# Kernel optimization log

Hardware: AMD Instinct MI355X
Metric: run time of the kernel (lower is better)

Reference implementation:

```python
import jax, jax.numpy as jnp
import numpy as np

N, E, B = 150000, 600000, 1024
F_IN, F_HID = 78, 312          # 78 * 2**output_dim_power_0(=2)
OUT_DIM = 128
L, VOCAB, EMB = 1000, 26, 128  # num_features_xt+1 = 26 embedding rows
NF, KS = 8, 8                  # 2**n_filters_power, 2**kernel_size_power
CONV_FLAT = NF * (EMB - KS + 1)  # 8*121 = 968
K_HOPS = 2
SLOPE = 0.01                   # torch leaky_relu default

def _lin(k, i, o):
    s = 1.0 / np.sqrt(i)
    kw, kb = jax.random.split(k)
    return (jax.random.uniform(kw, (i, o), jnp.float32, -s, s),
            jax.random.uniform(kb, (o,), jnp.float32, -s, s))

def setup_inputs() -> dict:
    key = jax.random.key(0)
    ks = jax.random.split(key, 12)
    x = jax.random.normal(ks[0], (N, F_IN), jnp.float32)
    edge_index = jax.random.randint(ks[1], (2, E), 0, N)
    batch = (jnp.arange(N) * B) // N            # sorted graph ids, all B graphs nonempty
    target = jax.random.randint(ks[2], (B, L), 0, VOCAB)
    sgc_w, sgc_b = _lin(ks[3], F_IN, F_HID)
    fcg1_w, fcg1_b = _lin(ks[4], F_HID, OUT_DIM)
    emb_table = jax.random.normal(ks[5], (VOCAB, EMB), jnp.float32)
    sc = 1.0 / np.sqrt(L * KS)
    conv_w = jax.random.uniform(ks[6], (NF, L, KS), jnp.float32, -sc, sc)  # OIW
    conv_b = jax.random.uniform(ks[7], (NF,), jnp.float32, -sc, sc)
    fcxt_w, fcxt_b = _lin(ks[8], CONV_FLAT, OUT_DIM)
    fc1_w, fc1_b = _lin(ks[9], 2 * OUT_DIM, 1024)
    fc2_w, fc2_b = _lin(ks[10], 1024, 512)
    out_w, out_b = _lin(ks[11], 512, 1)
    return dict(x=x, sgc_w=sgc_w, sgc_b=sgc_b, fcg1_w=fcg1_w, fcg1_b=fcg1_b,
                emb_table=emb_table, conv_w=conv_w, conv_b=conv_b,
                fcxt_w=fcxt_w, fcxt_b=fcxt_b, fc1_w=fc1_w, fc1_b=fc1_b,
                fc2_w=fc2_w, fc2_b=fc2_b, out_w=out_w, out_b=out_b,
                edge_index=edge_index, batch=batch, target=target)

def reference(x, sgc_w, sgc_b, fcg1_w, fcg1_b, emb_table, conv_w, conv_b,
              fcxt_w, fcxt_b, fc1_w, fc1_b, fc2_w, fc2_b, out_w, out_b,
              edge_index, batch, target):
    # --- SGConv: K-hop symmetric-normalized propagation with self-loops, then linear ---
    loop = jnp.arange(N)
    src = jnp.concatenate([edge_index[0], loop])
    dst = jnp.concatenate([edge_index[1], loop])
    deg = jax.ops.segment_sum(jnp.ones_like(src, jnp.float32), dst, num_segments=N)
    dinv = jnp.where(deg > 0, jax.lax.rsqrt(deg), 0.0)
    norm = (dinv[src] * dinv[dst])[:, None]
    h = x
    for _ in range(K_HOPS):
        h = jax.ops.segment_sum(h[src] * norm, dst, num_segments=N)  # [N, F]
    h = jax.nn.leaky_relu(h @ sgc_w + sgc_b, SLOPE)                  # [N, 312]
    # --- global max pool per graph + fc_g1 ---
    g = jax.ops.segment_max(h, batch, num_segments=B)                # [B, 312]
    g = jax.nn.leaky_relu(g @ fcg1_w + fcg1_b, SLOPE)                # [B, 128]
    # --- protein branch: embed -> Conv1d(in=1000) over embed axis -> flatten -> fc ---
    emb = emb_table[target]                                          # [B, 1000, 128]
    conv = jax.lax.conv_general_dilated(emb, conv_w, (1,), 'VALID',
                                        dimension_numbers=('NCW', 'OIW', 'NCW'))
    conv = conv + conv_b[None, :, None]                              # [B, 8, 121]
    xt = conv.reshape(B, CONV_FLAT) @ fcxt_w + fcxt_b                # [B, 128]
    # --- head ---
    xc = jnp.concatenate([g, xt], axis=1)                            # [B, 256]
    xc = jax.nn.relu(xc @ fc1_w + fc1_b)
    xc = jax.nn.relu(xc @ fc2_w + fc2_b)
    return xc @ out_w + out_b                                        # [B, 1]
```

## Files before the change

### kernel.cpp

```cpp
#include <hip/hip_runtime.h>

#define N_NODES 150000
#define N_EDGES 600000
#define BATCH   1024
#define F_IN    78
#define F_HID   312
#define OUT_DIMW 128
#define SEQ_L   1000
#define VOCAB   26
#define EMB     128
#define NF      8
#define KS      8
#define CONV_WO 121
#define CONV_FLAT 968
#define SK      208
#define SLOPE   0.01f
#define KEY_NEGMAX ((int)0x80800000)
#define SCAN_NBLK ((N_NODES + 255) / 256)

#define NT   20
#define BSW_HALF (3 * NT * 64 * 8)
#define M_PAD 150016
#define GM_BLKS (M_PAD / 128 * 2)
#define GM_CHUNK (GM_BLKS / 8)

#define WSW_HALF 65536

typedef __attribute__((ext_vector_type(8))) short bf8;
typedef __attribute__((ext_vector_type(4))) float f4;

__device__ __forceinline__ short f2bf(float f) {
  unsigned u = __float_as_uint(f);
  return (short)((u + 0x7fffu + ((u >> 16) & 1u)) >> 16);
}
__device__ __forceinline__ float bf2f(short h) {
  return __uint_as_float(((unsigned)(unsigned short)h) << 16);
}

__device__ __forceinline__ int fkey(float v) {
  int i = __float_as_int(v);
  return i >= 0 ? i : (i ^ 0x7fffffff);
}
__device__ __forceinline__ float fdec(int k) {
  return __int_as_float(k >= 0 ? k : (k ^ 0x7fffffff));
}

__global__ void k_zero_i(int* __restrict__ p, int n) {
  int i = blockIdx.x * blockDim.x + threadIdx.x;
  if (i < n) p[i] = 0;
}

__global__ void k_deg(const int* __restrict__ dst, int* __restrict__ deg) {
  int e = blockIdx.x * blockDim.x + threadIdx.x;
  if (e < N_EDGES) atomicAdd(&deg[dst[e]], 1);
}

__global__ void k_dinv(const int* __restrict__ deg, float* __restrict__ dinv) {
  int i = blockIdx.x * blockDim.x + threadIdx.x;
  if (i < N_NODES) dinv[i] = rsqrtf((float)(deg[i] + 1));
}

__global__ __launch_bounds__(256) void k_scan1(const int* __restrict__ deg, int* __restrict__ rowptr,
                                               int* __restrict__ bsum) {
  __shared__ int s[256];
  int tid = threadIdx.x;
  int i = blockIdx.x * 256 + tid;
  int v = (i < N_NODES) ? deg[i] : 0;
  s[tid] = v;
  __syncthreads();
  int x = v;
  for (int o = 1; o < 256; o <<= 1) {
    int t = (tid >= o) ? s[tid - o] : 0;
    __syncthreads();
    x += t; s[tid] = x;
    __syncthreads();
  }
  if (i < N_NODES) rowptr[i] = x - v;
  if (tid == 255) bsum[blockIdx.x] = x;
}

__global__ __launch_bounds__(1024) void k_scan2(int* __restrict__ bsum) {
  __shared__ int s[1024];
  int tid = threadIdx.x;
  int v = (tid < SCAN_NBLK) ? bsum[tid] : 0;
  s[tid] = v;
  __syncthreads();
  int x = v;
  for (int o = 1; o < 1024; o <<= 1) {
    int t = (tid >= o) ? s[tid - o] : 0;
    __syncthreads();
    x += t; s[tid] = x;
    __syncthreads();
  }
  if (tid < SCAN_NBLK) bsum[tid] = x - v;
}

__global__ __launch_bounds__(256) void k_scan3(int* __restrict__ rowptr, const int* __restrict__ bsum,
                                               int* __restrict__ cnt) {
  int i = blockIdx.x * 256 + threadIdx.x;
  if (i < N_NODES) { rowptr[i] += bsum[blockIdx.x]; cnt[i] = 0; }
  if (i == 0) rowptr[N_NODES] = N_EDGES;
}

__global__ void k_fillcsr(const int* __restrict__ src, const int* __restrict__ dst,
                          const int* __restrict__ rowptr, int* __restrict__ cnt,
                          int* __restrict__ csr) {
  int e = blockIdx.x * blockDim.x + threadIdx.x;
  if (e < N_EDGES) {
    int d = dst[e];
    int pos = rowptr[d] + atomicAdd(&cnt[d], 1);
    csr[pos] = src[e];
  }
}

template<int HOP1>
__global__ __launch_bounds__(256) void k_pull(const int* __restrict__ rowptr,
                        const int* __restrict__ csr, const float* __restrict__ dinv,
                        const float* __restrict__ p, void* __restrict__ outv) {
  int dv = (int)((blockIdx.x * 256 + threadIdx.x) >> 6);
  if (dv >= N_NODES) return;
  int d = __builtin_amdgcn_readfirstlane(dv);
  int lane = threadIdx.x & 63;
  int j0 = rowptr[d], j1 = rowptr[d + 1];
  bool act = lane < 39;
  float dd = dinv[d];
  float2 aA = make_float2(0.f, 0.f), aB = aA, aC = aA, aD = aA;
  if (act) {
    float2 v = ((const float2*)(p + (size_t)d * F_IN))[lane];
    float c0 = HOP1 ? dd : 1.f;
    aA.x = c0 * v.x; aA.y = c0 * v.y;
  }
  int j = j0;
  for (; j + 3 < j1; j += 4) {
    int s0 = csr[j], s1 = csr[j + 1], s2 = csr[j + 2], s3 = csr[j + 3];
    float c0 = HOP1 ? dinv[s0] : 1.f, c1 = HOP1 ? dinv[s1] : 1.f;
    float c2 = HOP1 ? dinv[s2] : 1.f, c3 = HOP1 ? dinv[s3] : 1.f;
    if (act) {
      float2 u0 = ((const float2*)(p + (size_t)s0 * F_IN))[lane];
      float2 u1 = ((const float2*)(p + (size_t)s1 * F_IN))[lane];
      float2 u2 = ((const float2*)(p + (size_t)s2 * F_IN))[lane];
      float2 u3 = ((const float2*)(p + (size_t)s3 * F_IN))[lane];
      aA.x += c0 * u0.x; aA.y += c0 * u0.y;
      aB.x += c1 * u1.x; aB.y += c1 * u1.y;
      aC.x += c2 * u2.x; aC.y += c2 * u2.y;
      aD.x += c3 * u3.x; aD.y += c3 * u3.y;
    }
  }
  if (j + 1 < j1) {
    int s0 = csr[j], s1 = csr[j + 1];
    float c0 = HOP1 ? dinv[s0] : 1.f, c1 = HOP1 ? dinv[s1] : 1.f;
    if (act) {
      float2 u0 = ((const float2*)(p + (size_t)s0 * F_IN))[lane];
      float2 u1 = ((const float2*)(p + (size_t)s1 * F_IN))[lane];
      aA.x += c0 * u0.x; aA.y += c0 * u0.y;
      aB.x += c1 * u1.x; aB.y += c1 * u1.y;
    }
    j += 2;
  }
  if (j < j1) {
    int s0 = csr[j];
    float c0 = HOP1 ? dinv[s0] : 1.f;
    if (act) {
      float2 u0 = ((const float2*)(p + (size_t)s0 * F_IN))[lane];
      aC.x += c0 * u0.x; aC.y += c0 * u0.y;
    }
  }
  if (HOP1) {
    if (act) {
      float cs = dd * dd;
      ((float2*)((float*)outv + (size_t)d * F_IN))[lane] =
          make_float2(cs * (aA.x + aB.x + aC.x + aD.x), cs * (aA.y + aB.y + aC.y + aD.y));
    }
  } else {
    if (lane < 48) {
      float vx = dd * (aA.x + aB.x + aC.x + aD.x);
      float vy = dd * (aA.y + aB.y + aC.y + aD.y);
      short hx = f2bf(vx); short lx = f2bf(vx - bf2f(hx));
      short hy = f2bf(vy); short ly = f2bf(vy - bf2f(hy));
      int t = d >> 4, mrow = d & 15;
      int ksi = lane >> 4;
      int quad = (lane & 15) >> 2;
      int jj = (2 * lane) & 7;
      size_t base = (((size_t)(t * 3 + ksi) * 2) * 64 + quad * 16 + mrow) * 8 + jj;
      short* o = (short*)outv;
      *(unsigned*)(o + base) =
          (unsigned)(unsigned short)hx | ((unsigned)(unsigned short)hy << 16);
      *(unsigned*)(o + base + 512) =
          (unsigned)(unsigned short)lx | ((unsigned)(unsigned short)ly << 16);
    }
  }
}

__global__ __launch_bounds__(256) void k_gemm_sk(const float* __restrict__ A, const float* __restrict__ B,
                        float* __restrict__ Cp, int M, int N, int K, int kc) {
  __shared__ float As[16][33];
  __shared__ float Bs[16][68];
  int bm = blockIdx.x * 32, bn = blockIdx.y * 64;
  int k0s = blockIdx.z * kc;
  int k1s = min(K, k0s + kc);
  int tid = threadIdx.x;
  int tx = tid & 15, ty = tid >> 4;
  float acc[2][4] = {};
  for (int k0 = k0s; k0 < k1s; k0 += 16) {
    {
      int i2 = tid * 2;
      int m = i2 >> 4, k = i2 & 15;
      float2 av = make_float2(0.f, 0.f);
      const float* Ap = A + (size_t)(bm + m) * K + k0 + k;
      if (k0 + k + 1 < k1s)      av = *(const float2*)Ap;
      else if (k0 + k < k1s)     av.x = Ap[0];
      As[k][m] = av.x; As[k + 1][m] = av.y;
    }
    {
      int i4 = tid * 4;
      int kr = i4 >> 6, n = i4 & 63;
      float4 bv = make_float4(0.f, 0.f, 0.f, 0.f);
      if (k0 + kr < k1s) bv = *(const float4*)(B + (size_t)(k0 + kr) * N + bn + n);
      *(float4*)&Bs[kr][n] = bv;
    }
    __syncthreads();
#pragma unroll
    for (int kk = 0; kk < 16; kk++) {
      float a0 = As[kk][ty * 2], a1 = As[kk][ty * 2 + 1];
      float4 b = *(const float4*)&Bs[kk][tx * 4];
      acc[0][0] += a0 * b.x; acc[0][1] += a0 * b.y; acc[0][2] += a0 * b.z; acc[0][3] += a0 * b.w;
      acc[1][0] += a1 * b.x; acc[1][1] += a1 * b.y; acc[1][2] += a1 * b.z; acc[1][3] += a1 * b.w;
    }
    __syncthreads();
  }
#pragma unroll
  for (int im = 0; im < 2; im++) {
    int m = bm + ty * 2 + im;
    float4 v = make_float4(acc[im][0], acc[im][1], acc[im][2], acc[im][3]);
    *(float4*)(Cp + ((size_t)blockIdx.z * M + m) * N + bn + tx * 4) = v;
  }
}

template<int ACT>
__global__ void k_sumact(const float* __restrict__ Cp, int S, const float* __restrict__ bias,
                         float* __restrict__ C, int nshift, int ldc, int coff) {
  int i = blockIdx.x * 256 + threadIdx.x;
  int MN = gridDim.x * 256;
  int m = i >> nshift, n = i & ((1 << nshift) - 1);
  float s = 0.f;
  for (int t = 0; t < S; t++) s += Cp[(size_t)t * MN + i];
  s += bias[n];
  if (ACT == 1) s = fmaxf(s, 0.f);
  if (ACT == 2) s = s > 0.f ? s : SLOPE * s;
  C[(size_t)m * ldc + coff + n] = s;
}

__global__ void k_bprep(const float* __restrict__ B, short* __restrict__ Bsw,
                        int* __restrict__ gkeys) {
  int i = blockIdx.x * 256 + threadIdx.x;
  if (i < BATCH * F_HID) gkeys[i] = KEY_NEGMAX;
  if (i >= BSW_HALF) return;
  int j = i & 7;
  int lane = (i >> 3) & 63;
  int rest = i >> 9;
  int nt = rest % NT, ksi = rest / NT;
  int n = nt * 16 + (lane & 15);
  int k = ksi * 32 + (lane >> 4) * 8 + j;
  float v = (k < F_IN && n < F_HID) ? B[k * F_HID + n] : 0.f;
  short h = f2bf(v);
  Bsw[i] = h;
  Bsw[BSW_HALF + i] = f2bf(v - bf2f(h));
}

__global__ void k_wprep(const float* __restrict__ conv_w, short* __restrict__ Wsw) {
  int i = blockIdx.x * 256 + threadIdx.x;
  if (i >= WSW_HALF) return;
  int j = i & 7;
  int lane = (i >> 3) & 63;
  int rest = i >> 9;
  int nt = rest & 3, ks = rest >> 2;
  int fk = nt * 16 + (lane & 15);
  int l = ks * 32 + (lane >> 4) * 8 + j;
  float v = (l < SEQ_L) ? conv_w[(fk >> 3) * (SEQ_L * KS) + l * KS + (fk & 7)] : 0.f;
  short h = f2bf(v);
  Wsw[i] = h;
  Wsw[WSW_HALF + i] = f2bf(v - bf2f(h));
}

__global__ __launch_bounds__(512) void k_gemm_max(const short* __restrict__ hA,
                           const short* __restrict__ Bsw,
                           const float* __restrict__ bias, int* __restrict__ gkeys) {
  __shared__ int red[2 * F_HID];
  int tid = threadIdx.x;

  int bid = blockIdx.x;
  int swz = (bid & 7) * GM_CHUNK + (bid >> 3);
  int mIdx = swz >> 1, nh2 = swz & 1;
  int m0 = mIdx * 128;

  int w = tid >> 6, lane = tid & 63;
  int mq = w & 3, nh = w >> 2;
  int ntb = (nh2 * 2 + nh) * 5;
  int mrow = lane & 15, quad = lane >> 4;

  int t0 = (m0 + mq * 32) >> 4;
  const short* apb = hA + (size_t)t0 * 3072 + (size_t)lane * 8;
  bf8 ah[2][3], al[2][3];
#pragma unroll
  for (int mi = 0; mi < 2; mi++)
#pragma unroll
    for (int ksi = 0; ksi < 3; ksi++) {
      const short* ap = apb + (size_t)(mi * 3 + ksi) * 1024;
      ah[mi][ksi] = *(const bf8*)ap;
      al[mi][ksi] = *(const bf8*)(ap + 512);
    }

  for (int i = tid; i < 2 * F_HID; i += 512) red[i] = KEY_NEGMAX;
  __syncthreads();

  f4 acc[2][5];
#pragma unroll
  for (int mi = 0; mi < 2; mi++)
#pragma unroll
    for (int j = 0; j < 5; j++) acc[mi][j] = (f4)0.f;

  const short* bbase = Bsw + ((size_t)ntb * 64 + lane) * 8;

#pragma unroll
  for (int ksi = 0; ksi < 3; ksi++) {
    const short* bh = bbase + (size_t)ksi * (NT * 512);
    const short* bl = bh + BSW_HALF;
#pragma unroll
    for (int j = 0; j < 5; j++) {
      bf8 bhv = *(const bf8*)(bh + j * 512);
      bf8 blv = *(const bf8*)(bl + j * 512);
#pragma unroll
      for (int mi = 0; mi < 2; mi++) {
        acc[mi][j] = __builtin_amdgcn_mfma_f32_16x16x32_bf16(ah[mi][ksi], bhv, acc[mi][j], 0, 0, 0);
        acc[mi][j] = __builtin_amdgcn_mfma_f32_16x16x32_bf16(al[mi][ksi], bhv, acc[mi][j], 0, 0, 0);
        acc[mi][j] = __builtin_amdgcn_mfma_f32_16x16x32_bf16(ah[mi][ksi], blv, acc[mi][j], 0, 0, 0);
      }
    }
  }

  int g0 = (int)(((long long)m0 * BATCH) / N_NODES);
#pragma unroll
  for (int mi = 0; mi < 2; mi++) {
    int mgrp = m0 + mq * 32 + mi * 16;
    int gg  = (int)(((long long)mgrp * BATCH) / N_NODES);
    int bndg = (int)((((long long)(gg + 1)) * N_NODES + BATCH - 1) / BATCH);
    int s = gg - g0;
    int mb = mgrp + quad * 4;
    if (bndg >= mgrp + 16 && mgrp + 16 <= N_NODES) {
#pragma unroll
      for (int j = 0; j < 5; j++) {
        int n = (ntb + j) * 16 + mrow;
        bool nok = n < F_HID;
        float bn = nok ? bias[n] : 0.f;
        float v0 = acc[mi][j][0] + bn; v0 = v0 > 0.f ? v0 : SLOPE * v0;
        float v1 = acc[mi][j][1] + bn; v1 = v1 > 0.f ? v1 : SLOPE * v1;
        float v2 = acc[mi][j][2] + bn; v2 = v2 > 0.f ? v2 : SLOPE * v2;
        float v3 = acc[mi][j][3] + bn; v3 = v3 > 0.f ? v3 : SLOPE * v3;
        float mx = fmaxf(fmaxf(v0, v1), fmaxf(v2, v3));
        mx = fmaxf(mx, __shfl_xor(mx, 16, 64));
        mx = fmaxf(mx, __shfl_xor(mx, 32, 64));
        if (quad == 0 && nok) atomicMax(&red[s * F_HID + n], fkey(mx));
      }
    } else {
#pragma unroll
      for (int j = 0; j < 5; j++) {
        int n = (ntb + j) * 16 + mrow;
        bool nok = n < F_HID;
        float bn = nok ? bias[n] : 0.f;
        float mx0 = -3.4e38f, mx1 = -3.4e38f;
#pragma unroll
        for (int r = 0; r < 4; r++) {
          int m = mb + r;
          if (m >= N_NODES) continue;
          float v = acc[mi][j][r] + bn;
          v = v > 0.f ? v : SLOPE * v;
          if (m >= bndg) mx1 = fmaxf(mx1, v); else mx0 = fmaxf(mx0, v);
        }
        mx0 = fmaxf(mx0, __shfl_xor(mx0, 16, 64));
        mx0 = fmaxf(mx0, __shfl_xor(mx0, 32, 64));
        mx1 = fmaxf(mx1, __shfl_xor(mx1, 16, 64));
        mx1 = fmaxf(mx1, __shfl_xor(mx1, 32, 64));
        if (quad == 0 && nok) {
          if (mx0 > -3.3e38f) atomicMax(&red[s * F_HID + n], fkey(mx0));
          if (mx1 > -3.3e38f && s == 0) atomicMax(&red[F_HID + n], fkey(mx1));
        }
      }
    }
  }
  __syncthreads();
  for (int i = tid; i < 2 * F_HID; i += 512) {
    int flag = i / F_HID, n = i - flag * F_HID;
    int g = g0 + flag;
    int key = red[i];
    if (g < BATCH && key != KEY_NEGMAX)
      atomicMax(&gkeys[g * F_HID + n], key);
  }
}

__global__ void k_decode(const int* __restrict__ gkeys, float* __restrict__ g, int n) {
  int i = blockIdx.x * blockDim.x + threadIdx.x;
  if (i < n) g[i] = fdec(gkeys[i]);
}

__global__ __launch_bounds__(256) void k_sbuild(const int* __restrict__ target,
                        const short* __restrict__ Wsw, float* __restrict__ Sg) {
  __shared__ int tl[4][1024];
  int tid = threadIdx.x;
  int w = tid >> 6, lane = tid & 63;
  int b = blockIdx.x * 4 + w;

  const int4* tg4 = (const int4*)(target + (size_t)b * SEQ_L);
  int4* tl4 = (int4*)&tl[w][0];
  for (int i = lane; i < 250; i += 64) tl4[i] = tg4[i];
  if (lane < 24) tl[w][1000 + lane] = -1;
  __syncthreads();

  int mrow = lane & 15, quad = lane >> 4;
  f4 acc[2][4];
#pragma unroll
  for (int mt = 0; mt < 2; mt++)
#pragma unroll
    for (int nt = 0; nt < 4; nt++) acc[mt][nt] = (f4)0.f;

  const short one = (short)0x3F80;
#pragma unroll 4
  for (int ks = 0; ks < 32; ks++) {
    int l0 = ks * 32 + quad * 8;
    int4 t0 = *(const int4*)&tl[w][l0];
    int4 t1 = *(const int4*)&tl[w][l0 + 4];
    int tv[8] = {t0.x, t0.y, t0.z, t0.w, t1.x, t1.y, t1.z, t1.w};
    bf8 a0, a1;
#pragma unroll
    for (int j = 0; j < 8; j++) {
      a0[j] = (tv[j] == mrow) ? one : (short)0;
      a1[j] = (tv[j] == mrow + 16) ? one : (short)0;
    }
    const short* bp = Wsw + ((size_t)(ks * 4) * 64 + lane) * 8;
    bf8 bh[4], bl[4];
#pragma unroll
    for (int nt = 0; nt < 4; nt++) {
      bh[nt] = *(const bf8*)(bp + nt * 512);
      bl[nt] = *(const bf8*)(bp + nt * 512 + WSW_HALF);
    }
#pragma unroll
    for (int nt = 0; nt < 4; nt++) {
      acc[0][nt] = __builtin_amdgcn_mfma_f32_16x16x32_bf16(a0, bh[nt], acc[0][nt], 0, 0, 0);
      acc[1][nt] = __builtin_amdgcn_mfma_f32_16x16x32_bf16(a1, bh[nt], acc[1][nt], 0, 0, 0);
    }
#pragma unroll
    for (int nt = 0; nt < 4; nt++) {
      acc[0][nt] = __builtin_amdgcn_mfma_f32_16x16x32_bf16(a0, bl[nt], acc[0][nt], 0, 0, 0);
      acc[1][nt] = __builtin_amdgcn_mfma_f32_16x16x32_bf16(a1, bl[nt], acc[1][nt], 0, 0, 0);
    }
  }

#pragma unroll
  for (int mt = 0; mt < 2; mt++)
#pragma unroll
    for (int nt = 0; nt < 4; nt++) {
      int fk = nt * 16 + mrow;
      float* sp = Sg + ((size_t)b * NF + (fk >> 3)) * SK + (fk & 7);
#pragma unroll
      for (int r = 0; r < 4; r++) {
        int v = mt * 16 + quad * 4 + r;
        if (v < VOCAB) sp[v * KS] = acc[mt][nt][r];
      }
    }
}

__global__ __launch_bounds__(256) void k_conv(const float* __restrict__ Sg, const float* __restrict__ emb,
                       const float* __restrict__ conv_b, float* __restrict__ convo) {
  __shared__ float Asub[32][SK];
  __shared__ float Etab[VOCAB * EMB];
  int r0 = blockIdx.x * 32;
  int tid = threadIdx.x;
  float* Af = &Asub[0][0];
  for (int i = tid; i < VOCAB * EMB; i += 256) Etab[i] = emb[i];
  for (int i = tid; i < 32 * SK; i += 256) Af[i] = Sg[(size_t)r0 * SK + i];
  __syncthreads();
  int w = tid & 127;
  int rg = tid >> 7;
  if (w < CONV_WO) {
    float acc[16] = {};
    for (int vk4 = 0; vk4 < SK; vk4 += 4) {
      int v0 = vk4 >> 3, k0 = vk4 & 7;
      float e0 = Etab[v0 * EMB + w + k0];
      float e1 = Etab[v0 * EMB + w + k0 + 1];
      float e2 = Etab[v0 * EMB + w + k0 + 2];
      float e3 = Etab[v0 * EMB + w + k0 + 3];
#pragma unroll
      for (int r = 0; r < 16; r++) {
        float4 a4 = *(const float4*)&Asub[rg * 16 + r][vk4];
        acc[r] += a4.x * e0 + a4.y * e1 + a4.z * e2 + a4.w * e3;
      }
    }
#pragma unroll
    for (int r = 0; r < 16; r++) {
      int row = r0 + rg * 16 + r;
      convo[(size_t)row * CONV_WO + w] = acc[r] + conv_b[row & 7];
    }
  }
}

__global__ void k_out(const float* __restrict__ a2, const float* __restrict__ w,
                      const float* __restrict__ b, float* __restrict__ out) {
  int row = (blockIdx.x * blockDim.x + threadIdx.x) >> 6;
  int lane = threadIdx.x & 63;
  if (row >= BATCH) return;
  const float* ar = a2 + (size_t)row * 512;
  float s = 0.f;
  for (int j = lane; j < 512; j += 64) s += ar[j] * w[j];
  for (int o = 32; o > 0; o >>= 1) s += __shfl_down(s, o, 64);
  if (lane == 0) out[row] = s + b[0];
}

extern "C" void kernel_launch(void* const* d_in, const int* in_sizes, int n_in,
                              void* d_out, int out_size, void* d_ws, size_t ws_size,
                              hipStream_t stream) {
  const float* x      = (const float*)d_in[0];
  const float* sgc_w  = (const float*)d_in[1];
  const float* sgc_b  = (const float*)d_in[2];
  const float* fcg1_w = (const float*)d_in[3];
  const float* fcg1_b = (const float*)d_in[4];
  const float* emb    = (const float*)d_in[5];
  const float* conv_w = (const float*)d_in[6];
  const float* conv_b = (const float*)d_in[7];
  const float* fcxt_w = (const float*)d_in[8];
  const float* fcxt_b = (const float*)d_in[9];
  const float* fc1_w  = (const float*)d_in[10];
  const float* fc1_b  = (const float*)d_in[11];
  const float* fc2_w  = (const float*)d_in[12];
  const float* fc2_b  = (const float*)d_in[13];
  const float* out_w  = (const float*)d_in[14];
  const float* out_b  = (const float*)d_in[15];
  const int* edge     = (const int*)d_in[16];
  const int* target   = (const int*)d_in[18];
  float* out = (float*)d_out;

  char* ws = (char*)d_ws;
  size_t off = 0;
  auto take = [&](size_t bytes) {
    void* p = ws + off;
    off += (bytes + 255) & ~(size_t)255;
    return p;
  };
  int*      deg    = (int*)     take((size_t)N_NODES * 4);
  float*    dinv   = (float*)   take((size_t)N_NODES * 4);
  int*      rowptr = (int*)     take((size_t)(N_NODES + 1) * 4);
  int*      bsum   = (int*)     take((size_t)SCAN_NBLK * 4);
  int*      cnt    = (int*)     take((size_t)N_NODES * 4);
  int*      csr    = (int*)     take((size_t)N_EDGES * 4);
  short*    hA     = (short*)   take((size_t)M_PAD * 192 * 2);
  float*    hB     = (float*)   take((size_t)N_NODES * F_IN * 4);
  short*    Bsw    = (short*)   take((size_t)2 * BSW_HALF * 2);
  short*    Wsw    = (short*)   take((size_t)2 * WSW_HALF * 2);
  int*      gkeys  = (int*)     take((size_t)BATCH * F_HID * 4);
  float*    gbuf   = (float*)   take((size_t)BATCH * F_HID * 4);
  float*    Sg     = (float*)   take((size_t)BATCH * NF * SK * 4);
  float*    convo  = (float*)   take((size_t)BATCH * NF * CONV_WO * 4);
  float*    xc     = (float*)   take((size_t)BATCH * 256 * 4);
  float*    a1     = (float*)   take((size_t)BATCH * 1024 * 4);
  float*    a2     = (float*)   take((size_t)BATCH * 512 * 4);
  float*    psum   = hB;

  const int* esrc = edge;
  const int* edst = edge + N_EDGES;

  k_zero_i<<<(N_NODES + 255) / 256, 256, 0, stream>>>(deg, N_NODES);
  k_deg<<<(N_EDGES + 255) / 256, 256, 0, stream>>>(edst, deg);
  k_dinv<<<(N_NODES + 255) / 256, 256, 0, stream>>>(deg, dinv);
  k_scan1<<<SCAN_NBLK, 256, 0, stream>>>(deg, rowptr, bsum);
  k_scan2<<<1, 1024, 0, stream>>>(bsum);
  k_scan3<<<SCAN_NBLK, 256, 0, stream>>>(rowptr, bsum, cnt);
  k_fillcsr<<<(N_EDGES + 255) / 256, 256, 0, stream>>>(esrc, edst, rowptr, cnt, csr);

  k_pull<1><<<(N_NODES * 64 + 255) / 256, 256, 0, stream>>>(rowptr, csr, dinv, x, hB);
  k_pull<0><<<(N_NODES * 64 + 255) / 256, 256, 0, stream>>>(rowptr, csr, dinv, hB, hA);

  k_bprep<<<(BATCH * F_HID + 255) / 256, 256, 0, stream>>>(sgc_w, Bsw, gkeys);
  k_gemm_max<<<GM_BLKS, 512, 0, stream>>>(hA, Bsw, sgc_b, gkeys);
  k_decode<<<(BATCH * F_HID + 255) / 256, 256, 0, stream>>>(gkeys, gbuf, BATCH * F_HID);

  {
    dim3 g(BATCH / 32, OUT_DIMW / 64, 4);
    k_gemm_sk<<<g, 256, 0, stream>>>(gbuf, fcg1_w, psum, BATCH, OUT_DIMW, F_HID, 80);
    k_sumact<2><<<(BATCH * OUT_DIMW) / 256, 256, 0, stream>>>(psum, 4, fcg1_b, xc, 7, 256, 0);
  }

  k_wprep<<<WSW_HALF / 256, 256, 0, stream>>>(conv_w, Wsw);
  k_sbuild<<<BATCH / 4, 256, 0, stream>>>(target, Wsw, Sg);
  k_conv<<<(BATCH * NF) / 32, 256, 0, stream>>>(Sg, emb, conv_b, convo);
  {
    dim3 g(BATCH / 32, OUT_DIMW / 64, 8);
    k_gemm_sk<<<g, 256, 0, stream>>>(convo, fcxt_w, psum, BATCH, OUT_DIMW, CONV_FLAT, 128);
    k_sumact<0><<<(BATCH * OUT_DIMW) / 256, 256, 0, stream>>>(psum, 8, fcxt_b, xc, 7, 256, OUT_DIMW);
  }

  {
    dim3 g(BATCH / 32, 1024 / 64, 2);
    k_gemm_sk<<<g, 256, 0, stream>>>(xc, fc1_w, psum, BATCH, 1024, 256, 128);
    k_sumact<1><<<(BATCH * 1024) / 256, 256, 0, stream>>>(psum, 2, fc1_b, a1, 10, 1024, 0);
  }
  {
    dim3 g(BATCH / 32, 512 / 64, 4);
    k_gemm_sk<<<g, 256, 0, stream>>>(a1, fc2_w, psum, BATCH, 512, 1024, 256);
    k_sumact<1><<<(BATCH * 512) / 256, 256, 0, stream>>>(psum, 4, fc2_b, a2, 9, 512, 0);
  }
  k_out<<<(BATCH * 64) / 256, 256, 0, stream>>>(a2, out_w, out_b, out);
}
```

Before: 494.7 us.

## Fuse small prep kernels, pad hop-1 rows, fold decode and fc1 bias/relu

```diff
diff --git a/kernel.cpp b/kernel.cpp
--- a/kernel.cpp
+++ b/kernel.cpp
@@ -4,6 +4,7 @@
 #define N_EDGES 600000
 #define BATCH   1024
 #define F_IN    78
+#define HB_S    80
 #define F_HID   312
 #define OUT_DIMW 128
 #define SEQ_L   1000
@@ -55,13 +56,8 @@
   if (e < N_EDGES) atomicAdd(&deg[dst[e]], 1);
 }
 
-__global__ void k_dinv(const int* __restrict__ deg, float* __restrict__ dinv) {
-  int i = blockIdx.x * blockDim.x + threadIdx.x;
-  if (i < N_NODES) dinv[i] = rsqrtf((float)(deg[i] + 1));
-}
-
 __global__ __launch_bounds__(256) void k_scan1(const int* __restrict__ deg, int* __restrict__ rowptr,
-                                               int* __restrict__ bsum) {
+                                               int* __restrict__ bsum, float* __restrict__ dinv) {
   __shared__ int s[256];
   int tid = threadIdx.x;
   int i = blockIdx.x * 256 + tid;
@@ -75,7 +71,10 @@
     x += t; s[tid] = x;
     __syncthreads();
   }
-  if (i < N_NODES) rowptr[i] = x - v;
+  if (i < N_NODES) {
+    rowptr[i] = x - v;
+    dinv[i] = rsqrtf((float)(v + 1));
+  }
   if (tid == 255) bsum[blockIdx.x] = x;
 }
 
@@ -117,6 +116,7 @@
 __global__ __launch_bounds__(256) void k_pull(const int* __restrict__ rowptr,
                         const int* __restrict__ csr, const float* __restrict__ dinv,
                         const float* __restrict__ p, void* __restrict__ outv) {
+  const int RS = HOP1 ? F_IN : HB_S;
   int dv = (int)((blockIdx.x * 256 + threadIdx.x) >> 6);
   if (dv >= N_NODES) return;
   int d = __builtin_amdgcn_readfirstlane(dv);
@@ -126,7 +126,7 @@
   float dd = dinv[d];
   float2 aA = make_float2(0.f, 0.f), aB = aA, aC = aA, aD = aA;
   if (act) {
-    float2 v = ((const float2*)(p + (size_t)d * F_IN))[lane];
+    float2 v = ((const float2*)(p + (size_t)d * RS))[lane];
     float c0 = HOP1 ? dd : 1.f;
     aA.x = c0 * v.x; aA.y = c0 * v.y;
   }
@@ -136,10 +136,10 @@
     float c0 = HOP1 ? dinv[s0] : 1.f, c1 = HOP1 ? dinv[s1] : 1.f;
     float c2 = HOP1 ? dinv[s2] : 1.f, c3 = HOP1 ? dinv[s3] : 1.f;
     if (act) {
-      float2 u0 = ((const float2*)(p + (size_t)s0 * F_IN))[lane];
-      float2 u1 = ((const float2*)(p + (size_t)s1 * F_IN))[lane];
-      float2 u2 = ((const float2*)(p + (size_t)s2 * F_IN))[lane];
-      float2 u3 = ((const float2*)(p + (size_t)s3 * F_IN))[lane];
+      float2 u0 = ((const float2*)(p + (size_t)s0 * RS))[lane];
+      float2 u1 = ((const float2*)(p + (size_t)s1 * RS))[lane];
+      float2 u2 = ((const float2*)(p + (size_t)s2 * RS))[lane];
+      float2 u3 = ((const float2*)(p + (size_t)s3 * RS))[lane];
       aA.x += c0 * u0.x; aA.y += c0 * u0.y;
       aB.x += c1 * u1.x; aB.y += c1 * u1.y;
       aC.x += c2 * u2.x; aC.y += c2 * u2.y;
@@ -150,8 +150,8 @@
     int s0 = csr[j], s1 = csr[j + 1];
     float c0 = HOP1 ? dinv[s0] : 1.f, c1 = HOP1 ? dinv[s1] : 1.f;
     if (act) {
-      float2 u0 = ((const float2*)(p + (size_t)s0 * F_IN))[lane];
-      float2 u1 = ((const float2*)(p + (size_t)s1 * F_IN))[lane];
+      float2 u0 = ((const float2*)(p + (size_t)s0 * RS))[lane];
+      float2 u1 = ((const float2*)(p + (size_t)s1 * RS))[lane];
       aA.x += c0 * u0.x; aA.y += c0 * u0.y;
       aB.x += c1 * u1.x; aB.y += c1 * u1.y;
     }
@@ -161,14 +161,14 @@
     int s0 = csr[j];
     float c0 = HOP1 ? dinv[s0] : 1.f;
     if (act) {
-      float2 u0 = ((const float2*)(p + (size_t)s0 * F_IN))[lane];
+      float2 u0 = ((const float2*)(p + (size_t)s0 * RS))[lane];
       aC.x += c0 * u0.x; aC.y += c0 * u0.y;
     }
   }
   if (HOP1) {
     if (act) {
       float cs = dd * dd;
-      ((float2*)((float*)outv + (size_t)d * F_IN))[lane] =
+      ((float2*)((float*)outv + (size_t)d * HB_S))[lane] =
           make_float2(cs * (aA.x + aB.x + aC.x + aD.x), cs * (aA.y + aB.y + aC.y + aD.y));
     }
   } else {
@@ -191,6 +191,7 @@
   }
 }
 
+template<int DEC>
 __global__ __launch_bounds__(256) void k_gemm_sk(const float* __restrict__ A, const float* __restrict__ B,
                         float* __restrict__ Cp, int M, int N, int K, int kc) {
   __shared__ float As[16][33];
@@ -209,6 +210,7 @@
       const float* Ap = A + (size_t)(bm + m) * K + k0 + k;
       if (k0 + k + 1 < k1s)      av = *(const float2*)Ap;
       else if (k0 + k < k1s)     av.x = Ap[0];
+      if (DEC) { av.x = fdec(__float_as_int(av.x)); av.y = fdec(__float_as_int(av.y)); }
       As[k][m] = av.x; As[k + 1][m] = av.y;
     }
     {
@@ -233,6 +235,54 @@
     int m = bm + ty * 2 + im;
     float4 v = make_float4(acc[im][0], acc[im][1], acc[im][2], acc[im][3]);
     *(float4*)(Cp + ((size_t)blockIdx.z * M + m) * N + bn + tx * 4) = v;
+  }
+}
+
+template<int ACT>
+__global__ __launch_bounds__(256) void k_gemm_dw(const float* __restrict__ A, const float* __restrict__ B,
+                        const float* __restrict__ bias, float* __restrict__ C, int M, int N, int K) {
+  __shared__ float As[16][33];
+  __shared__ float Bs[16][68];
+  int bm = blockIdx.x * 32, bn = blockIdx.y * 64;
+  int tid = threadIdx.x;
+  int tx = tid & 15, ty = tid >> 4;
+  float acc[2][4] = {};
+  for (int k0 = 0; k0 < K; k0 += 16) {
+    {
+      int i2 = tid * 2;
+      int m = i2 >> 4, k = i2 & 15;
+      float2 av = make_float2(0.f, 0.f);
+      const float* Ap = A + (size_t)(bm + m) * K + k0 + k;
+      if (k0 + k + 1 < K)      av = *(const float2*)Ap;
+      else if (k0 + k < K)     av.x = Ap[0];
+      As[k][m] = av.x; As[k + 1][m] = av.y;
+    }
+    {
+      int i4 = tid * 4;
+      int kr = i4 >> 6, n = i4 & 63;
+      float4 bv = make_float4(0.f, 0.f, 0.f, 0.f);
+      if (k0 + kr < K) bv = *(const float4*)(B + (size_t)(k0 + kr) * N + bn + n);
+      *(float4*)&Bs[kr][n] = bv;
+    }
+    __syncthreads();
+#pragma unroll
+    for (int kk = 0; kk < 16; kk++) {
+      float a0 = As[kk][ty * 2], a1 = As[kk][ty * 2 + 1];
+      float4 b = *(const float4*)&Bs[kk][tx * 4];
+      acc[0][0] += a0 * b.x; acc[0][1] += a0 * b.y; acc[0][2] += a0 * b.z; acc[0][3] += a0 * b.w;
+      acc[1][0] += a1 * b.x; acc[1][1] += a1 * b.y; acc[1][2] += a1 * b.z; acc[1][3] += a1 * b.w;
+    }
+    __syncthreads();
+  }
+  float4 bv = *(const float4*)&bias[bn + tx * 4];
+#pragma unroll
+  for (int im = 0; im < 2; im++) {
+    int m = bm + ty * 2 + im;
+    float4 v = make_float4(acc[im][0] + bv.x, acc[im][1] + bv.y, acc[im][2] + bv.z, acc[im][3] + bv.w);
+    if (ACT == 1) { v.x = fmaxf(v.x, 0.f); v.y = fmaxf(v.y, 0.f); v.z = fmaxf(v.z, 0.f); v.w = fmaxf(v.w, 0.f); }
+    if (ACT == 2) { v.x = v.x > 0.f ? v.x : SLOPE * v.x; v.y = v.y > 0.f ? v.y : SLOPE * v.y;
+                    v.z = v.z > 0.f ? v.z : SLOPE * v.z; v.w = v.w > 0.f ? v.w : SLOPE * v.w; }
+    *(float4*)(C + (size_t)m * N + bn + tx * 4) = v;
   }
 }
 
@@ -250,36 +300,35 @@
   C[(size_t)m * ldc + coff + n] = s;
 }
 
-__global__ void k_bprep(const float* __restrict__ B, short* __restrict__ Bsw,
-                        int* __restrict__ gkeys) {
+__global__ void k_prep(const float* __restrict__ B, short* __restrict__ Bsw,
+                       const float* __restrict__ conv_w, short* __restrict__ Wsw,
+                       int* __restrict__ gkeys) {
   int i = blockIdx.x * 256 + threadIdx.x;
   if (i < BATCH * F_HID) gkeys[i] = KEY_NEGMAX;
-  if (i >= BSW_HALF) return;
-  int j = i & 7;
-  int lane = (i >> 3) & 63;
-  int rest = i >> 9;
-  int nt = rest % NT, ksi = rest / NT;
-  int n = nt * 16 + (lane & 15);
-  int k = ksi * 32 + (lane >> 4) * 8 + j;
-  float v = (k < F_IN && n < F_HID) ? B[k * F_HID + n] : 0.f;
-  short h = f2bf(v);
-  Bsw[i] = h;
-  Bsw[BSW_HALF + i] = f2bf(v - bf2f(h));
-}
-
-__global__ void k_wprep(const float* __restrict__ conv_w, short* __restrict__ Wsw) {
-  int i = blockIdx.x * 256 + threadIdx.x;
-  if (i >= WSW_HALF) return;
-  int j = i & 7;
-  int lane = (i >> 3) & 63;
-  int rest = i >> 9;
-  int nt = rest & 3, ks = rest >> 2;
-  int fk = nt * 16 + (lane & 15);
-  int l = ks * 32 + (lane >> 4) * 8 + j;
-  float v = (l < SEQ_L) ? conv_w[(fk >> 3) * (SEQ_L * KS) + l * KS + (fk & 7)] : 0.f;
-  short h = f2bf(v);
-  Wsw[i] = h;
-  Wsw[WSW_HALF + i] = f2bf(v - bf2f(h));
+  if (i < BSW_HALF) {
+    int j = i & 7;
+    int lane = (i >> 3) & 63;
+    int rest = i >> 9;
+    int nt = rest % NT, ksi = rest / NT;
+    int n = nt * 16 + (lane & 15);
+    int k = ksi * 32 + (lane >> 4) * 8 + j;
+    float v = (k < F_IN && n < F_HID) ? B[k * F_HID + n] : 0.f;
+    short h = f2bf(v);
+    Bsw[i] = h;
+    Bsw[BSW_HALF + i] = f2bf(v - bf2f(h));
+  }
+  if (i < WSW_HALF) {
+    int j = i & 7;
+    int lane = (i >> 3) & 63;
+    int rest = i >> 9;
+    int nt = rest & 3, ks = rest >> 2;
+    int fk = nt * 16 + (lane & 15);
+    int l = ks * 32 + (lane >> 4) * 8 + j;
+    float v = (l < SEQ_L) ? conv_w[(fk >> 3) * (SEQ_L * KS) + l * KS + (fk & 7)] : 0.f;
+    short h = f2bf(v);
+    Wsw[i] = h;
+    Wsw[WSW_HALF + i] = f2bf(v - bf2f(h));
+  }
 }
 
 __global__ __launch_bounds__(512) void k_gemm_max(const short* __restrict__ hA,
@@ -395,11 +444,6 @@
     if (g < BATCH && key != KEY_NEGMAX)
       atomicMax(&gkeys[g * F_HID + n], key);
   }
-}
-
-__global__ void k_decode(const int* __restrict__ gkeys, float* __restrict__ g, int n) {
-  int i = blockIdx.x * blockDim.x + threadIdx.x;
-  if (i < n) g[i] = fdec(gkeys[i]);
 }
 
 __global__ __launch_bounds__(256) void k_sbuild(const int* __restrict__ target,
@@ -551,11 +595,10 @@
   int*      cnt    = (int*)     take((size_t)N_NODES * 4);
   int*      csr    = (int*)     take((size_t)N_EDGES * 4);
   short*    hA     = (short*)   take((size_t)M_PAD * 192 * 2);
-  float*    hB     = (float*)   take((size_t)N_NODES * F_IN * 4);
+  float*    hB     = (float*)   take((size_t)N_NODES * HB_S * 4);
   short*    Bsw    = (short*)   take((size_t)2 * BSW_HALF * 2);
   short*    Wsw    = (short*)   take((size_t)2 * WSW_HALF * 2);
   int*      gkeys  = (int*)     take((size_t)BATCH * F_HID * 4);
-  float*    gbuf   = (float*)   take((size_t)BATCH * F_HID * 4);
   float*    Sg     = (float*)   take((size_t)BATCH * NF * SK * 4);
   float*    convo  = (float*)   take((size_t)BATCH * NF * CONV_WO * 4);
   float*    xc     = (float*)   take((size_t)BATCH * 256 * 4);
@@ -568,42 +611,39 @@
 
   k_zero_i<<<(N_NODES + 255) / 256, 256, 0, stream>>>(deg, N_NODES);
   k_deg<<<(N_EDGES + 255) / 256, 256, 0, stream>>>(edst, deg);
-  k_dinv<<<(N_NODES + 255) / 256, 256, 0, stream>>>(deg, dinv);
-  k_scan1<<<SCAN_NBLK, 256, 0, stream>>>(deg, rowptr, bsum);
+  k_scan1<<<SCAN_NBLK, 256, 0, stream>>>(deg, rowptr, bsum, dinv);
   k_scan2<<<1, 1024, 0, stream>>>(bsum);
   k_scan3<<<SCAN_NBLK, 256, 0, stream>>>(rowptr, bsum, cnt);
   k_fillcsr<<<(N_EDGES + 255) / 256, 256, 0, stream>>>(esrc, edst, rowptr, cnt, csr);
 
+  k_prep<<<(BATCH * F_HID + 255) / 256, 256, 0, stream>>>(sgc_w, Bsw, conv_w, Wsw, gkeys);
+
   k_pull<1><<<(N_NODES * 64 + 255) / 256, 256, 0, stream>>>(rowptr, csr, dinv, x, hB);
   k_pull<0><<<(N_NODES * 64 + 255) / 256, 256, 0, stream>>>(rowptr, csr, dinv, hB, hA);
 
-  k_bprep<<<(BATCH * F_HID + 255) / 256, 256, 0, stream>>>(sgc_w, Bsw, gkeys);
   k_gemm_max<<<GM_BLKS, 512, 0, stream>>>(hA, Bsw, sgc_b, gkeys);
-  k_decode<<<(BATCH * F_HID + 255) / 256, 256, 0, stream>>>(gkeys, gbuf, BATCH * F_HID);
 
   {
     dim3 g(BATCH / 32, OUT_DIMW / 64, 4);
-    k_gemm_sk<<<g, 256, 0, stream>>>(gbuf, fcg1_w, psum, BATCH, OUT_DIMW, F_HID, 80);
+    k_gemm_sk<1><<<g, 256, 0, stream>>>((const float*)gkeys, fcg1_w, psum, BATCH, OUT_DIMW, F_HID, 80);
     k_sumact<2><<<(BATCH * OUT_DIMW) / 256, 256, 0, stream>>>(psum, 4, fcg1_b, xc, 7, 256, 0);
   }
 
-  k_wprep<<<WSW_HALF / 256, 256, 0, stream>>>(conv_w, Wsw);
   k_sbuild<<<BATCH / 4, 256, 0, stream>>>(target, Wsw, Sg);
   k_conv<<<(BATCH * NF) / 32, 256, 0, stream>>>(Sg, emb, conv_b, convo);
   {
     dim3 g(BATCH / 32, OUT_DIMW / 64, 8);
-    k_gemm_sk<<<g, 256, 0, stream>>>(convo, fcxt_w, psum, BATCH, OUT_DIMW, CONV_FLAT, 128);
+    k_gemm_sk<0><<<g, 256, 0, stream>>>(convo, fcxt_w, psum, BATCH, OUT_DIMW, CONV_FLAT, 128);
     k_sumact<0><<<(BATCH * OUT_DIMW) / 256, 256, 0, stream>>>(psum, 8, fcxt_b, xc, 7, 256, OUT_DIMW);
   }
 
   {
-    dim3 g(BATCH / 32, 1024 / 64, 2);
-    k_gemm_sk<<<g, 256, 0, stream>>>(xc, fc1_w, psum, BATCH, 1024, 256, 128);
-    k_sumact<1><<<(BATCH * 1024) / 256, 256, 0, stream>>>(psum, 2, fc1_b, a1, 10, 1024, 0);
+    dim3 g(BATCH / 32, 1024 / 64);
+    k_gemm_dw<1><<<g, 256, 0, stream>>>(xc, fc1_w, fc1_b, a1, BATCH, 1024, 256);
   }
   {
     dim3 g(BATCH / 32, 512 / 64, 4);
-    k_gemm_sk<<<g, 256, 0, stream>>>(a1, fc2_w, psum, BATCH, 512, 1024, 256);
+    k_gemm_sk<0><<<g, 256, 0, stream>>>(a1, fc2_w, psum, BATCH, 512, 1024, 256);
     k_sumact<1><<<(BATCH * 512) / 256, 256, 0, stream>>>(psum, 4, fc2_b, a2, 9, 512, 0);
   }
   k_out<<<(BATCH * 64) / 256, 256, 0, stream>>>(a2, out_w, out_b, out);
```

New measurement: 482.6 us. -2.5%, faster.
